# Kernel tuning notes

Hardware: AMD Instinct MI355X
Metric: run time of the kernel (lower is better)

The kernel has to match this reference:

```python
import jax, jax.numpy as jnp
import numpy as np

L, B, C, H = 577, 8, 768, 12
HD = C // H
SCALE = HD ** -0.5
EPS = 1e-5


def layer_norm(x, g, b):
    # fp32 LN (matches the fp16-safe LayerNorm subclass)
    x32 = x.astype(jnp.float32)
    mu = jnp.mean(x32, axis=-1, keepdims=True)
    var = jnp.var(x32, axis=-1, keepdims=True)
    return ((x32 - mu) * jax.lax.rsqrt(var + EPS) * g + b).astype(x.dtype)


def quick_gelu(x):
    return x * jax.nn.sigmoid(1.702 * x)


def mlp(x, ln2_g, ln2_b, fc_w, fc_b, cproj_w, cproj_b):
    h = quick_gelu(layer_norm(x, ln2_g, ln2_b) @ fc_w.T + fc_b)
    return h @ cproj_w.T + cproj_b


def v2v_attention(x, qkv_w, qkv_b, proj_w, proj_b):
    # x: [B, N, C]
    Bb, N, Cc = x.shape
    qkv = (x @ qkv_w.T + qkv_b).reshape(Bb, N, 3, H, HD).transpose(2, 0, 3, 1, 4)
    q, k, v = qkv[0], qkv[1], qkv[2]  # [B, H, N, hd]
    attn_ori = jax.nn.softmax(jnp.einsum('bhid,bhjd->bhij', q, k) * SCALE, axis=-1)
    # v2v: k = v, q = k (settings='')
    attn = jax.nn.softmax(jnp.einsum('bhid,bhjd->bhij', v, v) * SCALE, axis=-1)
    xo = jnp.einsum('bhij,bhjd->bhid', attn, v).transpose(0, 2, 1, 3).reshape(Bb, N, Cc)
    xori = jnp.einsum('bhij,bhjd->bhid', attn_ori, v).transpose(0, 2, 1, 3).reshape(Bb, N, Cc)
    return xo @ proj_w.T + proj_b, xori @ proj_w.T + proj_b


def setup_inputs() -> dict:
    key = jax.random.key(0)
    ks = jax.random.split(key, 10)
    s = 0.02
    return {
        'x_res': jax.random.normal(ks[0], (L, B, C), jnp.float32),
        'x': jax.random.normal(ks[1], (L, B, C), jnp.float32),
        'ln1_g': jnp.ones((C,), jnp.float32),
        'ln1_b': jnp.zeros((C,), jnp.float32),
        'ln2_g': jnp.ones((C,), jnp.float32),
        'ln2_b': jnp.zeros((C,), jnp.float32),
        'qkv_w': jax.random.normal(ks[2], (3 * C, C), jnp.float32) * s,
        'qkv_b': jnp.zeros((3 * C,), jnp.float32),
        'proj_w': jax.random.normal(ks[3], (C, C), jnp.float32) * s,
        'proj_b': jnp.zeros((C,), jnp.float32),
        'fc_w': jax.random.normal(ks[4], (4 * C, C), jnp.float32) * s,
        'fc_b': jnp.zeros((4 * C,), jnp.float32),
        'cproj_w': jax.random.normal(ks[5], (C, 4 * C), jnp.float32) * s,
        'cproj_b': jnp.zeros((C,), jnp.float32),
    }


def reference(x_res, x, ln1_g, ln1_b, ln2_g, ln2_b, qkv_w, qkv_b, proj_w, proj_b, fc_w, fc_b, cproj_w, cproj_b):
    # x, x_res: [L, B, C] (seq-first)
    y = layer_norm(x, ln1_g, ln1_b).transpose(1, 0, 2)  # [B, L, C]
    y = y @ qkv_w.T + qkv_b                              # [B, L, 3C]
    Bb, Ll, C3 = y.shape
    y = y.reshape(Bb, Ll, 3, C3 // 3).transpose(2, 0, 1, 3).reshape(3 * Bb, Ll, C3 // 3)
    y = y @ proj_w.T + proj_b                            # [3B, L, C]
    q, k, v = jnp.split(y, 3, axis=0)
    q = q.transpose(1, 0, 2)  # [L, B, C]
    k = k.transpose(1, 0, 2)
    v = v.transpose(1, 0, 2)
    v = v + x
    v = v + mlp(v, ln2_g, ln2_b, fc_w, fc_b, cproj_w, cproj_b)
    xa = layer_norm(x.transpose(1, 0, 2), ln1_g, ln1_b)  # [B, L, C]
    x_res_out, x_ori_res = v2v_attention(xa, qkv_w, qkv_b, proj_w, proj_b)
    x_res_out = x_res_out.transpose(1, 0, 2)
    x_ori_res = x_ori_res.transpose(1, 0, 2)
    x = x + x_ori_res
    x = x + mlp(x, ln2_g, ln2_b, fc_w, fc_b, cproj_w, cproj_b)
    x_res = x_res + x_res_out
    return (x, q, k, v, x_res)
```

## Files before the change

### kernel.cpp

```cpp
#include <hip/hip_runtime.h>
#include <math.h>

#define L_SEQ 577
#define BATCH 8
#define CDIM  768
#define NHEAD 12
#define ROWS  (L_SEQ * BATCH)
#define LBC   ((size_t)ROWS * CDIM)

typedef __attribute__((ext_vector_type(8))) short bf16x8;
typedef __attribute__((ext_vector_type(4))) float f32x4;

enum { EPI_NONE = 0, EPI_ADD = 1, EPI_GELU = 2 };

__device__ __forceinline__ ushort f2bf(float f) {
  unsigned u = __float_as_uint(f);
  u += 0x7fffu + ((u >> 16) & 1u);
  return (ushort)(u >> 16);
}

__device__ __forceinline__ void gload16(const void* g, void* l) {
  __builtin_amdgcn_global_load_lds(
      (const __attribute__((address_space(1))) unsigned int*)g,
      (__attribute__((address_space(3))) unsigned int*)l, 16, 0, 0);
}

__device__ __forceinline__ float wave_sum(float v) {
#pragma unroll
  for (int o = 32; o > 0; o >>= 1) v += __shfl_xor(v, o);
  return v;
}

__global__ __launch_bounds__(256) void cast_bf16(const float* __restrict__ in,
                                                 ushort* __restrict__ out, int n4) {
  int i = blockIdx.x * blockDim.x + threadIdx.x;
  const int stride = gridDim.x * blockDim.x;
  for (; i < n4; i += stride) {
    float4 v = ((const float4*)in)[i];
    ushort4 o;
    o.x = f2bf(v.x); o.y = f2bf(v.y); o.z = f2bf(v.z); o.w = f2bf(v.w);
    ((ushort4*)out)[i] = o;
  }
}

__global__ __launch_bounds__(256) void ln_kernel(
    const float* __restrict__ x, const float* __restrict__ g,
    const float* __restrict__ bta, ushort* __restrict__ out, int rows)
{
  const int wave = threadIdx.x >> 6, lane = threadIdx.x & 63;
  const int r = blockIdx.x * 4 + wave;
  if (r >= rows) return;
  const float4* xr = (const float4*)(x + (size_t)r * CDIM);
  float4 v[3];
  float s = 0.f, s2 = 0.f;
#pragma unroll
  for (int j = 0; j < 3; ++j) {
    v[j] = xr[lane + 64 * j];
    s  += v[j].x + v[j].y + v[j].z + v[j].w;
    s2 += v[j].x * v[j].x + v[j].y * v[j].y + v[j].z * v[j].z + v[j].w * v[j].w;
  }
  s = wave_sum(s); s2 = wave_sum(s2);
  const float mu = s * (1.f / 768.f);
  const float var = s2 * (1.f / 768.f) - mu * mu;
  const float rs = rsqrtf(var + 1e-5f);
  ushort4* orow = (ushort4*)(out + (size_t)r * CDIM);
#pragma unroll
  for (int j = 0; j < 3; ++j) {
    const int c4 = lane + 64 * j;
    const float4 gv = ((const float4*)g)[c4];
    const float4 bv = ((const float4*)bta)[c4];
    ushort4 o;
    o.x = f2bf((v[j].x - mu) * rs * gv.x + bv.x);
    o.y = f2bf((v[j].y - mu) * rs * gv.y + bv.y);
    o.z = f2bf((v[j].z - mu) * rs * gv.z + bv.z);
    o.w = f2bf((v[j].w - mu) * rs * gv.w + bv.w);
    orow[c4] = o;
  }
}

template <int BM, int BN, int WM, int WN, int EPI, bool OBF>
__global__ __launch_bounds__(256) void mfma_gemm(
    const ushort* __restrict__ A, int lda,
    const ushort* __restrict__ W, int K,
    const float* __restrict__ bias,
    void* __restrict__ Cp, int ldc,
    const float* __restrict__ res, int ldr, int M)
{
  constexpr int BK = 32;
  __shared__ short As[BM * BK];
  __shared__ short Bs[BN * BK];
  const int t = threadIdx.x;
  const int wv = t >> 6, ln = t & 63;
  const int m0 = blockIdx.x * BM, n0 = blockIdx.y * BN;
  constexpr int NWM = BM / WM;
  const int wm = wv % NWM, wn = wv / NWM;
  constexpr int MF = WM / 16, NF = WN / 16;
  const int mbase = wm * WM, nbase = wn * WN;
  const int srow = ln >> 2;
  const int schunk = ln & 3;
  const int lrow15 = ln & 15;
  const int kchunk = (ln >> 4) * 8;

  f32x4 acc[MF][NF] = {};

  for (int k0 = 0; k0 < K; k0 += BK) {
    __syncthreads();
#pragma unroll
    for (int q = 0; q < BM / 64; ++q) {
      const int row = q * 64 + wv * 16 + srow;
      int grow = m0 + row; if (grow > M - 1) grow = M - 1;
      gload16(A + (size_t)grow * lda + k0 + schunk * 8,
              &As[(q * 64 + wv * 16) * BK]);
    }
#pragma unroll
    for (int q = 0; q < BN / 64; ++q) {
      const int row = q * 64 + wv * 16 + srow;
      gload16(W + (size_t)(n0 + row) * K + k0 + schunk * 8,
              &Bs[(q * 64 + wv * 16) * BK]);
    }
    __syncthreads();
    bf16x8 af[MF], wf[NF];
#pragma unroll
    for (int i = 0; i < MF; ++i)
      af[i] = *(const bf16x8*)&As[(mbase + i * 16 + lrow15) * BK + kchunk];
#pragma unroll
    for (int j = 0; j < NF; ++j)
      wf[j] = *(const bf16x8*)&Bs[(nbase + j * 16 + lrow15) * BK + kchunk];
#pragma unroll
    for (int i = 0; i < MF; ++i)
#pragma unroll
      for (int j = 0; j < NF; ++j)
        acc[i][j] = __builtin_amdgcn_mfma_f32_16x16x32_bf16(wf[j], af[i], acc[i][j], 0, 0, 0);
  }

  const int nq = (ln >> 4) * 4;
#pragma unroll
  for (int i = 0; i < MF; ++i) {
    const int m = m0 + mbase + i * 16 + lrow15;
    if (m >= M) continue;
#pragma unroll
    for (int j = 0; j < NF; ++j) {
      const int n = n0 + nbase + j * 16 + nq;
      const float4 bv = *(const float4*)&bias[n];
      float o0 = acc[i][j][0] + bv.x;
      float o1 = acc[i][j][1] + bv.y;
      float o2 = acc[i][j][2] + bv.z;
      float o3 = acc[i][j][3] + bv.w;
      if (EPI == EPI_GELU) {
        o0 = o0 / (1.f + __expf(-1.702f * o0));
        o1 = o1 / (1.f + __expf(-1.702f * o1));
        o2 = o2 / (1.f + __expf(-1.702f * o2));
        o3 = o3 / (1.f + __expf(-1.702f * o3));
      }
      if (EPI == EPI_ADD) {
        const float4 rv = *(const float4*)&res[(size_t)m * ldr + n];
        o0 += rv.x; o1 += rv.y; o2 += rv.z; o3 += rv.w;
      }
      if (OBF) {
        ushort4 ov;
        ov.x = f2bf(o0); ov.y = f2bf(o1); ov.z = f2bf(o2); ov.w = f2bf(o3);
        *(ushort4*)((ushort*)Cp + (size_t)m * ldc + n) = ov;
      } else {
        *(float4*)((float*)Cp + (size_t)m * ldc + n) = make_float4(o0, o1, o2, o3);
      }
    }
  }
}

__global__ __launch_bounds__(256) void attn_kernel(
    const ushort* __restrict__ qkv,
    ushort* __restrict__ xo,
    ushort* __restrict__ xori)
{
  __shared__ short Ks[64 * 72];
  __shared__ short Vs[64 * 72];
  __shared__ short Vt[64 * 72];
  __shared__ short Ps[4][16 * 72];
  const int t = threadIdx.x;
  const int w = t >> 6, l = t & 63;
  const int b = blockIdx.y / NHEAD, h = blockIdx.y - (blockIdx.y / NHEAD) * NHEAD;
  const int q0 = blockIdx.x * 64;
  const int hoff = h * 64;
  const int l15 = l & 15, l16 = l >> 4;

  const int qrow0 = q0 + w * 16 + l15;
  const int qrow = qrow0 < L_SEQ ? qrow0 : (L_SEQ - 1);
  const size_t qbase = (size_t)(qrow * BATCH + b) * 2304 + hoff;
  bf16x8 qf[2][2];
#pragma unroll
  for (int ks = 0; ks < 2; ++ks) {
    qf[0][ks] = *(const bf16x8*)(qkv + qbase + 0    + ks * 32 + l16 * 8);
    qf[1][ks] = *(const bf16x8*)(qkv + qbase + 1536 + ks * 32 + l16 * 8);
  }

  float mS[2] = {-1e30f, -1e30f};
  float lS[2] = {0.f, 0.f};
  f32x4 accO[2][4] = {};

  const int sr = t >> 3;
  const int sc = (t & 7) * 8;

  for (int j0 = 0; j0 < 640; j0 += 64) {
    __syncthreads();
#pragma unroll
    for (int rep = 0; rep < 2; ++rep) {
      const int r = rep * 32 + sr;
      const int jl = j0 + r;
      const int jr = jl < L_SEQ ? jl : (L_SEQ - 1);
      const size_t gb = (size_t)(jr * BATCH + b) * 2304 + hoff + sc;
      const uint4 kv = *(const uint4*)(qkv + gb + 768);
      const uint4 vv = *(const uint4*)(qkv + gb + 1536);
      *(uint4*)&Ks[r * 72 + sc] = kv;
      *(uint4*)&Vs[r * 72 + sc] = vv;
      const ushort* vp = (const ushort*)&vv;
#pragma unroll
      for (int e = 0; e < 8; ++e)
        Vt[(sc + e) * 72 + (r ^ sc)] = vp[e];
    }
    __syncthreads();

#pragma unroll
    for (int att = 0; att < 2; ++att) {
      const short* keys = att ? Vs : Ks;
      f32x4 S[4] = {};
#pragma unroll
      for (int ks = 0; ks < 2; ++ks)
#pragma unroll
        for (int f = 0; f < 4; ++f) {
          const bf16x8 kf = *(const bf16x8*)&keys[(f * 16 + l15) * 72 + ks * 32 + l16 * 8];
          S[f] = __builtin_amdgcn_mfma_f32_16x16x32_bf16(kf, qf[att][ks], S[f], 0, 0, 0);
        }

      float tmax = -1e30f;
#pragma unroll
      for (int f = 0; f < 4; ++f)
#pragma unroll
        for (int r = 0; r < 4; ++r) {
          float s = S[f][r] * 0.125f;
          if (j0 + f * 16 + l16 * 4 + r >= L_SEQ) s = -1e30f;
          S[f][r] = s;
          tmax = fmaxf(tmax, s);
        }
      tmax = fmaxf(tmax, __shfl_xor(tmax, 16));
      tmax = fmaxf(tmax, __shfl_xor(tmax, 32));
      const float mold = mS[att];
      const float mnew = fmaxf(mold, tmax);
      const float corr = __expf(mold - mnew);
      mS[att] = mnew;

      float tsum = 0.f;
#pragma unroll
      for (int f = 0; f < 4; ++f) {
        ushort pb[4];
#pragma unroll
        for (int r = 0; r < 4; ++r) {
          const float p = __expf(S[f][r] - mnew);
          tsum += p;
          pb[r] = f2bf(p);
        }
        uint2 pk;
        pk.x = (unsigned)pb[0] | ((unsigned)pb[1] << 16);
        pk.y = (unsigned)pb[2] | ((unsigned)pb[3] << 16);
        *(uint2*)&Ps[w][l15 * 72 + f * 16 + l16 * 4] = pk;
      }
      tsum += __shfl_xor(tsum, 16);
      tsum += __shfl_xor(tsum, 32);
      lS[att] = lS[att] * corr + tsum;

      float corr4[4];
#pragma unroll
      for (int r = 0; r < 4; ++r) corr4[r] = __shfl(corr, l16 * 4 + r);
#pragma unroll
      for (int df = 0; df < 4; ++df)
#pragma unroll
        for (int r = 0; r < 4; ++r) accO[att][df][r] *= corr4[r];

#pragma unroll
      for (int ks = 0; ks < 2; ++ks) {
        const bf16x8 pf = *(const bf16x8*)&Ps[w][l15 * 72 + ks * 32 + l16 * 8];
#pragma unroll
        for (int df = 0; df < 4; ++df) {
          const int d = df * 16 + l15;
          const int s8 = (d >> 3) * 8;
          const bf16x8 vf = *(const bf16x8*)&Vt[d * 72 + ((ks * 32 + l16 * 8) ^ s8)];
          accO[att][df] = __builtin_amdgcn_mfma_f32_16x16x32_bf16(pf, vf, accO[att][df], 0, 0, 0);
        }
      }
    }
  }

#pragma unroll
  for (int att = 0; att < 2; ++att) {
    const float linv = 1.f / lS[att];
    float r4[4];
#pragma unroll
    for (int r = 0; r < 4; ++r) r4[r] = __shfl(linv, l16 * 4 + r);
    ushort* dst = att ? xo : xori;
#pragma unroll
    for (int r = 0; r < 4; ++r) {
      const int qq = q0 + w * 16 + l16 * 4 + r;
      if (qq < L_SEQ) {
        ushort* orow = dst + (size_t)(qq * BATCH + b) * CDIM + hoff + l15;
#pragma unroll
        for (int df = 0; df < 4; ++df)
          orow[df * 16] = f2bf(accO[att][df][r] * r4[r]);
      }
    }
  }
}

extern "C" void kernel_launch(void* const* d_in, const int* in_sizes, int n_in,
                              void* d_out, int out_size, void* d_ws, size_t ws_size,
                              hipStream_t stream)
{
  const float* x_res  = (const float*)d_in[0];
  const float* x      = (const float*)d_in[1];
  const float* ln1_g  = (const float*)d_in[2];
  const float* ln1_b  = (const float*)d_in[3];
  const float* ln2_g  = (const float*)d_in[4];
  const float* ln2_b  = (const float*)d_in[5];
  const float* qkv_w  = (const float*)d_in[6];
  const float* qkv_b  = (const float*)d_in[7];
  const float* proj_w = (const float*)d_in[8];
  const float* proj_b = (const float*)d_in[9];
  const float* fc_w   = (const float*)d_in[10];
  const float* fc_b   = (const float*)d_in[11];
  const float* cproj_w= (const float*)d_in[12];
  const float* cproj_b= (const float*)d_in[13];

  float* out_x  = (float*)d_out;
  float* out_q  = out_x + LBC;
  float* out_k  = out_x + 2 * LBC;
  float* out_v  = out_x + 3 * LBC;
  float* out_xr = out_x + 4 * LBC;

  ushort* wsQKVH = (ushort*)d_ws;
  ushort* wsLN   = wsQKVH + (size_t)ROWS * 3072;
  ushort* wsXO   = wsLN + LBC;
  ushort* wsXORI = wsXO + LBC;
  ushort* wQKVW  = wsXORI + LBC;
  ushort* wPROJ  = wQKVW + (size_t)2304 * 768;
  ushort* wFC    = wPROJ + (size_t)768 * 768;
  ushort* wCPROJ = wFC + (size_t)3072 * 768;

  const dim3 blk(256);

  cast_bf16<<<1024, blk, 0, stream>>>(qkv_w,  wQKVW,  2304 * 768 / 4);
  cast_bf16<<<1024, blk, 0, stream>>>(proj_w, wPROJ,  768 * 768 / 4);
  cast_bf16<<<1024, blk, 0, stream>>>(fc_w,   wFC,    3072 * 768 / 4);
  cast_bf16<<<1024, blk, 0, stream>>>(cproj_w, wCPROJ, 768 * 3072 / 4);

  ln_kernel<<<dim3((ROWS + 3) / 4), blk, 0, stream>>>(x, ln1_g, ln1_b, wsLN, ROWS);

  mfma_gemm<128,128,64,64,EPI_NONE,true><<<dim3(37, 18), blk, 0, stream>>>(
      wsLN, CDIM, wQKVW, CDIM, qkv_b, wsQKVH, 2304, nullptr, 0, ROWS);

  mfma_gemm<64,128,32,64,EPI_NONE,false><<<dim3(73, 6), blk, 0, stream>>>(
      wsQKVH + 0,    2304, wPROJ, CDIM, proj_b, out_q, CDIM, nullptr, 0, ROWS);
  mfma_gemm<64,128,32,64,EPI_NONE,false><<<dim3(73, 6), blk, 0, stream>>>(
      wsQKVH + 768,  2304, wPROJ, CDIM, proj_b, out_k, CDIM, nullptr, 0, ROWS);
  mfma_gemm<64,128,32,64,EPI_ADD,false><<<dim3(73, 6), blk, 0, stream>>>(
      wsQKVH + 1536, 2304, wPROJ, CDIM, proj_b, out_v, CDIM, x, CDIM, ROWS);

  attn_kernel<<<dim3(10, 96), blk, 0, stream>>>(wsQKVH, wsXO, wsXORI);

  mfma_gemm<64,128,32,64,EPI_ADD,false><<<dim3(73, 6), blk, 0, stream>>>(
      wsXO,   CDIM, wPROJ, CDIM, proj_b, out_xr, CDIM, x_res, CDIM, ROWS);
  mfma_gemm<64,128,32,64,EPI_ADD,false><<<dim3(73, 6), blk, 0, stream>>>(
      wsXORI, CDIM, wPROJ, CDIM, proj_b, out_x, CDIM, x, CDIM, ROWS);

  ln_kernel<<<dim3((ROWS + 3) / 4), blk, 0, stream>>>(out_v, ln2_g, ln2_b, wsLN, ROWS);
  mfma_gemm<128,128,64,64,EPI_GELU,true><<<dim3(37, 24), blk, 0, stream>>>(
      wsLN, CDIM, wFC, CDIM, fc_b, wsQKVH, 3072, nullptr, 0, ROWS);
  mfma_gemm<64,128,32,64,EPI_ADD,false><<<dim3(73, 6), blk, 0, stream>>>(
      wsQKVH, 3072, wCPROJ, 3072, cproj_b, out_v, CDIM, out_v, CDIM, ROWS);

  ln_kernel<<<dim3((ROWS + 3) / 4), blk, 0, stream>>>(out_x, ln2_g, ln2_b, wsLN, ROWS);
  mfma_gemm<128,128,64,64,EPI_GELU,true><<<dim3(37, 24), blk, 0, stream>>>(
      wsLN, CDIM, wFC, CDIM, fc_b, wsQKVH, 3072, nullptr, 0, ROWS);
  mfma_gemm<64,128,32,64,EPI_ADD,false><<<dim3(73, 6), blk, 0, stream>>>(
      wsQKVH, 3072, wCPROJ, 3072, cproj_b, out_x, CDIM, out_x, CDIM, ROWS);
}
```

Before: 560.1 us.

## Batch independent GEMMs and LNs into grouped launches with XCD-aware tile remap

Merges the three q/k/v projection GEMMs, the two attention-output projections, the two MLP branches (LN, FC and c_proj) into single launches using a z-dimension or concatenated rows. All GEMMs now use 128x128 tiles, and the workgroup index is remapped so that consecutive tiles land on the same XCD for better L2 reuse. This cuts launch count and fills the GPU better on small grids. In exchange, the workspace grows to hold two MLP hidden buffers, and 128-row tiles waste some work at the M tail.

```diff
diff --git a/kernel.cpp b/kernel.cpp
--- a/kernel.cpp
+++ b/kernel.cpp
@@ -10,8 +10,6 @@
 
 typedef __attribute__((ext_vector_type(8))) short bf16x8;
 typedef __attribute__((ext_vector_type(4))) float f32x4;
-
-enum { EPI_NONE = 0, EPI_ADD = 1, EPI_GELU = 2 };
 
 __device__ __forceinline__ ushort f2bf(float f) {
   unsigned u = __float_as_uint(f);
@@ -44,13 +42,16 @@
 }
 
 __global__ __launch_bounds__(256) void ln_kernel(
-    const float* __restrict__ x, const float* __restrict__ g,
-    const float* __restrict__ bta, ushort* __restrict__ out, int rows)
+    const float* __restrict__ srcA, const float* __restrict__ srcB,
+    const float* __restrict__ g, const float* __restrict__ bta,
+    ushort* __restrict__ out, int rowsTotal, int rowsPer)
 {
   const int wave = threadIdx.x >> 6, lane = threadIdx.x & 63;
   const int r = blockIdx.x * 4 + wave;
-  if (r >= rows) return;
-  const float4* xr = (const float4*)(x + (size_t)r * CDIM);
+  if (r >= rowsTotal) return;
+  const float4* xr = (r < rowsPer)
+      ? (const float4*)(srcA + (size_t)r * CDIM)
+      : (const float4*)(srcB + (size_t)(r - rowsPer) * CDIM);
   float4 v[3];
   float s = 0.f, s2 = 0.f;
 #pragma unroll
@@ -78,90 +79,101 @@
   }
 }
 
-template <int BM, int BN, int WM, int WN, int EPI, bool OBF>
+template <bool GELU, bool OBF>
 __global__ __launch_bounds__(256) void mfma_gemm(
-    const ushort* __restrict__ A, int lda,
+    const ushort* __restrict__ A, int lda, size_t a_zoff,
     const ushort* __restrict__ W, int K,
     const float* __restrict__ bias,
-    void* __restrict__ Cp, int ldc,
-    const float* __restrict__ res, int ldr, int M)
+    void* __restrict__ C0, void* __restrict__ C1, void* __restrict__ C2, int ldc,
+    const float* __restrict__ R0, const float* __restrict__ R1,
+    const float* __restrict__ R2, int ldr, int M)
 {
-  constexpr int BK = 32;
+  constexpr int BM = 128, BN = 128, BK = 32;
   __shared__ short As[BM * BK];
   __shared__ short Bs[BN * BK];
   const int t = threadIdx.x;
   const int wv = t >> 6, ln = t & 63;
-  const int m0 = blockIdx.x * BM, n0 = blockIdx.y * BN;
-  constexpr int NWM = BM / WM;
-  const int wm = wv % NWM, wn = wv / NWM;
-  constexpr int MF = WM / 16, NF = WN / 16;
-  const int mbase = wm * WM, nbase = wn * WN;
+
+  const int nwg = gridDim.x * gridDim.y;
+  const int orig = blockIdx.x + gridDim.x * blockIdx.y;
+  const int qq = nwg >> 3, rr = nwg & 7;
+  const int xcd = orig & 7, lid = orig >> 3;
+  const int wg = (xcd < rr ? xcd * (qq + 1) : rr * (qq + 1) + (xcd - rr) * qq) + lid;
+  const int m0 = (wg % gridDim.x) * BM, n0 = (wg / gridDim.x) * BN;
+
+  const int z = blockIdx.z;
+  const ushort* Az = A + (size_t)z * a_zoff;
+  void* Cv = z == 0 ? C0 : (z == 1 ? C1 : C2);
+  const float* res = z == 0 ? R0 : (z == 1 ? R1 : R2);
+
+  const int wm = wv & 1, wn = wv >> 1;
+  const int mbase = wm * 64, nbase = wn * 64;
   const int srow = ln >> 2;
   const int schunk = ln & 3;
   const int lrow15 = ln & 15;
   const int kchunk = (ln >> 4) * 8;
 
-  f32x4 acc[MF][NF] = {};
+  f32x4 acc[4][4] = {};
 
   for (int k0 = 0; k0 < K; k0 += BK) {
     __syncthreads();
 #pragma unroll
-    for (int q = 0; q < BM / 64; ++q) {
+    for (int q = 0; q < 2; ++q) {
       const int row = q * 64 + wv * 16 + srow;
       int grow = m0 + row; if (grow > M - 1) grow = M - 1;
-      gload16(A + (size_t)grow * lda + k0 + schunk * 8,
+      gload16(Az + (size_t)grow * lda + k0 + schunk * 8,
               &As[(q * 64 + wv * 16) * BK]);
     }
 #pragma unroll
-    for (int q = 0; q < BN / 64; ++q) {
+    for (int q = 0; q < 2; ++q) {
       const int row = q * 64 + wv * 16 + srow;
       gload16(W + (size_t)(n0 + row) * K + k0 + schunk * 8,
               &Bs[(q * 64 + wv * 16) * BK]);
     }
     __syncthreads();
-    bf16x8 af[MF], wf[NF];
-#pragma unroll
-    for (int i = 0; i < MF; ++i)
+    bf16x8 af[4], wf[4];
+#pragma unroll
+    for (int i = 0; i < 4; ++i)
       af[i] = *(const bf16x8*)&As[(mbase + i * 16 + lrow15) * BK + kchunk];
 #pragma unroll
-    for (int j = 0; j < NF; ++j)
+    for (int j = 0; j < 4; ++j)
       wf[j] = *(const bf16x8*)&Bs[(nbase + j * 16 + lrow15) * BK + kchunk];
 #pragma unroll
-    for (int i = 0; i < MF; ++i)
-#pragma unroll
-      for (int j = 0; j < NF; ++j)
+    for (int i = 0; i < 4; ++i)
+#pragma unroll
+      for (int j = 0; j < 4; ++j)
         acc[i][j] = __builtin_amdgcn_mfma_f32_16x16x32_bf16(wf[j], af[i], acc[i][j], 0, 0, 0);
   }
 
   const int nq = (ln >> 4) * 4;
 #pragma unroll
-  for (int i = 0; i < MF; ++i) {
+  for (int i = 0; i < 4; ++i) {
     const int m = m0 + mbase + i * 16 + lrow15;
     if (m >= M) continue;
 #pragma unroll
-    for (int j = 0; j < NF; ++j) {
+    for (int j = 0; j < 4; ++j) {
       const int n = n0 + nbase + j * 16 + nq;
       const float4 bv = *(const float4*)&bias[n];
       float o0 = acc[i][j][0] + bv.x;
       float o1 = acc[i][j][1] + bv.y;
       float o2 = acc[i][j][2] + bv.z;
       float o3 = acc[i][j][3] + bv.w;
-      if (EPI == EPI_GELU) {
+      if (GELU) {
         o0 = o0 / (1.f + __expf(-1.702f * o0));
         o1 = o1 / (1.f + __expf(-1.702f * o1));
         o2 = o2 / (1.f + __expf(-1.702f * o2));
         o3 = o3 / (1.f + __expf(-1.702f * o3));
       }
-      if (EPI == EPI_ADD) {
+      if (res) {
         const float4 rv = *(const float4*)&res[(size_t)m * ldr + n];
         o0 += rv.x; o1 += rv.y; o2 += rv.z; o3 += rv.w;
       }
       if (OBF) {
         ushort4 ov;
         ov.x = f2bf(o0); ov.y = f2bf(o1); ov.z = f2bf(o2); ov.w = f2bf(o3);
-        *(ushort4*)((ushort*)Cp + (size_t)m * ldc + n) = ov;
+        *(ushort4*)((ushort*)Cv + (size_t)m * ldc + n) = ov;
       } else {
-        *(float4*)((float*)Cp + (size_t)m * ldc + n) = make_float4(o0, o1, o2, o3);
+        *(float4*)((float*)Cv + (size_t)m * ldc + n) = make_float4(o0, o1, o2, o3);
       }
     }
   }
@@ -334,11 +346,11 @@
   float* out_v  = out_x + 3 * LBC;
   float* out_xr = out_x + 4 * LBC;
 
-  ushort* wsQKVH = (ushort*)d_ws;
-  ushort* wsLN   = wsQKVH + (size_t)ROWS * 3072;
-  ushort* wsXO   = wsLN + LBC;
+  ushort* wsH    = (ushort*)d_ws;
+  ushort* wsXO   = wsH + (size_t)ROWS * 2304;
   ushort* wsXORI = wsXO + LBC;
-  ushort* wQKVW  = wsXORI + LBC;
+  ushort* wsLN   = wsH + (size_t)2 * ROWS * 3072;
+  ushort* wQKVW  = wsLN + 2 * LBC;
   ushort* wPROJ  = wQKVW + (size_t)2304 * 768;
   ushort* wFC    = wPROJ + (size_t)768 * 768;
   ushort* wCPROJ = wFC + (size_t)3072 * 768;
@@ -350,34 +362,36 @@
   cast_bf16<<<1024, blk, 0, stream>>>(fc_w,   wFC,    3072 * 768 / 4);
   cast_bf16<<<1024, blk, 0, stream>>>(cproj_w, wCPROJ, 768 * 3072 / 4);
 
-  ln_kernel<<<dim3((ROWS + 3) / 4), blk, 0, stream>>>(x, ln1_g, ln1_b, wsLN, ROWS);
-
-  mfma_gemm<128,128,64,64,EPI_NONE,true><<<dim3(37, 18), blk, 0, stream>>>(
-      wsLN, CDIM, wQKVW, CDIM, qkv_b, wsQKVH, 2304, nullptr, 0, ROWS);
-
-  mfma_gemm<64,128,32,64,EPI_NONE,false><<<dim3(73, 6), blk, 0, stream>>>(
-      wsQKVH + 0,    2304, wPROJ, CDIM, proj_b, out_q, CDIM, nullptr, 0, ROWS);
-  mfma_gemm<64,128,32,64,EPI_NONE,false><<<dim3(73, 6), blk, 0, stream>>>(
-      wsQKVH + 768,  2304, wPROJ, CDIM, proj_b, out_k, CDIM, nullptr, 0, ROWS);
-  mfma_gemm<64,128,32,64,EPI_ADD,false><<<dim3(73, 6), blk, 0, stream>>>(
-      wsQKVH + 1536, 2304, wPROJ, CDIM, proj_b, out_v, CDIM, x, CDIM, ROWS);
-
-  attn_kernel<<<dim3(10, 96), blk, 0, stream>>>(wsQKVH, wsXO, wsXORI);
-
-  mfma_gemm<64,128,32,64,EPI_ADD,false><<<dim3(73, 6), blk, 0, stream>>>(
-      wsXO,   CDIM, wPROJ, CDIM, proj_b, out_xr, CDIM, x_res, CDIM, ROWS);
-  mfma_gemm<64,128,32,64,EPI_ADD,false><<<dim3(73, 6), blk, 0, stream>>>(
-      wsXORI, CDIM, wPROJ, CDIM, proj_b, out_x, CDIM, x, CDIM, ROWS);
-
-  ln_kernel<<<dim3((ROWS + 3) / 4), blk, 0, stream>>>(out_v, ln2_g, ln2_b, wsLN, ROWS);
-  mfma_gemm<128,128,64,64,EPI_GELU,true><<<dim3(37, 24), blk, 0, stream>>>(
-      wsLN, CDIM, wFC, CDIM, fc_b, wsQKVH, 3072, nullptr, 0, ROWS);
-  mfma_gemm<64,128,32,64,EPI_ADD,false><<<dim3(73, 6), blk, 0, stream>>>(
-      wsQKVH, 3072, wCPROJ, 3072, cproj_b, out_v, CDIM, out_v, CDIM, ROWS);
-
-  ln_kernel<<<dim3((ROWS + 3) / 4), blk, 0, stream>>>(out_x, ln2_g, ln2_b, wsLN, ROWS);
-  mfma_gemm<128,128,64,64,EPI_GELU,true><<<dim3(37, 24), blk, 0, stream>>>(
-      wsLN, CDIM, wFC, CDIM, fc_b, wsQKVH, 3072, nullptr, 0, ROWS);
-  mfma_gemm<64,128,32,64,EPI_ADD,false><<<dim3(73, 6), blk, 0, stream>>>(
-      wsQKVH, 3072, wCPROJ, 3072, cproj_b, out_x, CDIM, out_x, CDIM, ROWS);
-}
+  ln_kernel<<<dim3((ROWS + 3) / 4), blk, 0, stream>>>(
+      x, x, ln1_g, ln1_b, wsLN, ROWS, ROWS);
+
+  mfma_gemm<false, true><<<dim3(37, 18, 1), blk, 0, stream>>>(
+      wsLN, CDIM, 0, wQKVW, CDIM, qkv_b,
+      wsH, nullptr, nullptr, 2304,
+      nullptr, nullptr, nullptr, 0, ROWS);
+
+  mfma_gemm<false, false><<<dim3(37, 6, 3), blk, 0, stream>>>(
+      wsH, 2304, 768, wPROJ, CDIM, proj_b,
+      out_q, out_k, out_v, CDIM,
+      nullptr, nullptr, x, CDIM, ROWS);
+
+  attn_kernel<<<dim3(10, 96), blk, 0, stream>>>(wsH, wsXO, wsXORI);
+
+  mfma_gemm<false, false><<<dim3(37, 6, 2), blk, 0, stream>>>(
+      wsXO, CDIM, LBC, wPROJ, CDIM, proj_b,
+      out_xr, out_x, nullptr, CDIM,
+      x_res, x, nullptr, CDIM, ROWS);
+
+  ln_kernel<<<dim3((2 * ROWS + 3) / 4), blk, 0, stream>>>(
+      out_v, out_x, ln2_g, ln2_b, wsLN, 2 * ROWS, ROWS);
+
+  mfma_gemm<true, true><<<dim3(73, 24, 1), blk, 0, stream>>>(
+      wsLN, CDIM, 0, wFC, CDIM, fc_b,
+      wsH, nullptr, nullptr, 3072,
+      nullptr, nullptr, nullptr, 0, 2 * ROWS);
+
+  mfma_gemm<false, false><<<dim3(37, 6, 2), blk, 0, stream>>>(
+      wsH, 3072, (size_t)ROWS * 3072, wCPROJ, 3072, cproj_b,
+      out_v, out_x, nullptr, CDIM,
+      out_v, out_x, nullptr, CDIM, ROWS);
+}
```

Measured after the change: 498.3 us. 1.12x faster.
